# Kernel tuning notes

Measured on AMD Instinct MI355X. Metric: run time of the kernel, lower is better.

The kernel has to match this reference:

```python
import jax, jax.numpy as jnp
import numpy as np

NB = 4096      # num_batch
NUM = 128      # trajectory samples (P rows)
NVAR = 16      # polynomial coeffs (P cols)
NOBS = 10      # obstacles
NL, NU = 4, 8  # num_lower, num_upper
NPART = NU - NL
T_FIN = 10.0
A_OBS, B_OBS = 6.0, 3.2
RHO_INEQ = RHO_OBS = RHO_LANE = 1.0
V_MIN, V_MAX, A_MAX = 0.1, 30.0, 18.0
MAXITER = 30
W_SM = 100.0


def setup_inputs() -> dict:
    key = jax.random.key(0)
    ks = jax.random.split(key, 13)
    f = jnp.float32
    return {
        'P': jax.random.normal(ks[0], (NUM, NVAR), f),
        'Pdot': jax.random.normal(ks[1], (NUM, NVAR), f),
        'Pddot': jax.random.normal(ks[2], (NUM, NVAR), f),
        'init_state_ego': jax.random.normal(ks[3], (NB, 4), f),
        'fin_state_ego': jax.random.normal(ks[4], (NB, 3), f),
        'closest_obs': jax.random.normal(ks[5], (NB, 2 * NOBS), f),
        'v_obs': jax.random.normal(ks[6], (NB, 2 * NOBS), f),
        'y_ub': jax.random.uniform(ks[7], (NB,), f),
        'y_lb': jax.random.normal(ks[8], (NB,), f),
        'lamda_x': jax.random.normal(ks[9], (NB, NVAR), f),
        'lamda_y': jax.random.normal(ks[10], (NB, NVAR), f),
        'c_x_partial': jax.random.normal(ks[11], (NB, NPART), f),
        'c_y_partial': jax.random.normal(ks[12], (NB, NPART), f),
    }


def _forward(P, Pdot, Pddot, init_state_ego, fin_state_ego, closest_obs, v_obs,
             y_ub, y_lb, lamda_x, lamda_y, c_x_partial, c_y_partial):
    num, nvar = P.shape
    tot_time = jnp.linspace(0.0, T_FIN, num)
    eye = jnp.eye(nvar, dtype=P.dtype)
    A_part = eye[NL:NU]
    A_eq_x = jnp.vstack([P[0], Pdot[0], Pddot[0], Pdot[-1], A_part])            # [4+NPART, nvar]
    A_eq_y = jnp.vstack([P[0], Pdot[0], Pddot[0], P[-1], Pdot[-1], A_part])     # [5+NPART, nvar]
    cost_sm = W_SM * (Pddot.T @ Pddot + 0.1 * eye)
    A_vel, A_acc = Pdot, Pddot
    A_obs_mat = jnp.tile(P, (NOBS, 1))            # [NOBS*num, nvar]
    A_lane = jnp.vstack([P, -P])                  # [2*num, nvar]

    def kkt_inv(cost, A_eq):
        m = A_eq.shape[0]
        top = jnp.hstack([cost, A_eq.T])
        bot = jnp.hstack([A_eq, jnp.zeros((m, m), cost.dtype)])
        return jnp.linalg.inv(jnp.vstack([top, bot]))

    # --- obstacle trajectories: [B, NOBS*num] ---
    x_obs = closest_obs[:, :NOBS]; y_obs = closest_obs[:, NOBS:2 * NOBS]
    vx_obs = v_obs[:, :NOBS];      vy_obs = v_obs[:, NOBS:2 * NOBS]
    x_obs_traj = (x_obs[:, :, None] + vx_obs[:, :, None] * tot_time).reshape(NB, NOBS * num)
    y_obs_traj = (y_obs[:, :, None] + vy_obs[:, :, None] * tot_time).reshape(NB, NOBS * num)

    # --- boundary vectors ---
    x_init = init_state_ego[:, 0:1]; y_init = init_state_ego[:, 1:2]
    v_init = init_state_ego[:, 2:3]; psi_init = init_state_ego[:, 3:4]
    vx_init = v_init * jnp.cos(psi_init); vy_init = v_init * jnp.sin(psi_init)
    zc = jnp.zeros((NB, 1), P.dtype)
    x_fin = fin_state_ego[:, 0:1]; y_fin = fin_state_ego[:, 1:2]
    vx_fin = jnp.clip(fin_state_ego[:, 2:3], V_MIN, V_MAX)  # computed as in original (unused in b_eq)
    b_eq_x = jnp.hstack([x_init, vx_init, zc, x_fin, c_x_partial])
    b_eq_y = jnp.hstack([y_init, vy_init, zc, y_fin, zc, c_y_partial])

    # --- initialization QP (lincost = 0) ---
    cmi_x0 = kkt_inv(cost_sm, A_eq_x)
    cmi_y0 = kkt_inv(cost_sm, A_eq_y)
    sol_x0 = jnp.hstack([jnp.zeros((NB, nvar), P.dtype), b_eq_x]) @ cmi_x0.T
    sol_y0 = jnp.hstack([jnp.zeros((NB, nvar), P.dtype), b_eq_y]) @ cmi_y0.T
    primal_sol = jnp.hstack([sol_x0[:, :nvar], sol_y0[:, :nvar]])

    # --- optimizer KKT inverses ---
    cost_x = cost_sm + RHO_INEQ * (A_acc.T @ A_acc) + RHO_INEQ * (A_vel.T @ A_vel) + RHO_OBS * (A_obs_mat.T @ A_obs_mat)
    cost_y = cost_x + RHO_LANE * (A_lane.T @ A_lane)
    cmi_x = kkt_inv(cost_x, A_eq_x)
    cmi_y = kkt_inv(cost_y, A_eq_y)

    ones_num = jnp.ones((NB, num), P.dtype)
    b_lane = jnp.hstack([y_ub[:, None] * ones_num, -y_lb[:, None] * ones_num])  # [B, 2*num]

    def step(carry, _):
        primal, lx, ly = carry
        cx, cy = primal[:, :nvar], primal[:, nvar:]
        x, xdot, xddot = cx @ P.T, cx @ Pdot.T, cx @ Pddot.T      # [B, num]
        y, ydot, yddot = cy @ P.T, cy @ Pdot.T, cy @ Pddot.T

        wc = jnp.tile(x, (1, NOBS)) - x_obs_traj                   # [B, NOBS*num]
        ws = jnp.tile(y, (1, NOBS)) - y_obs_traj
        alpha_obs = jnp.arctan2(ws * A_OBS, wc * B_OBS)
        co, so = jnp.cos(alpha_obs), jnp.sin(alpha_obs)
        c1 = RHO_OBS * (A_OBS ** 2 * co ** 2 + B_OBS ** 2 * so ** 2)
        c2 = RHO_OBS * (A_OBS * wc * co + B_OBS * ws * so)
        d_obs = jnp.maximum(1.0, c2 / c1)

        alpha_v = jnp.arctan2(ydot, xdot)
        cv, sv = jnp.cos(alpha_v), jnp.sin(alpha_v)
        d_v = jnp.clip(RHO_INEQ * (xdot * cv + ydot * sv) / (RHO_INEQ * (cv ** 2 + sv ** 2)), V_MIN, V_MAX)

        alpha_a = jnp.arctan2(yddot, xddot)
        ca, sa = jnp.cos(alpha_a), jnp.sin(alpha_a)
        d_a = jnp.clip(RHO_INEQ * (xddot * ca + yddot * sa) / (RHO_INEQ * (ca ** 2 + sa ** 2)), 0.0, A_MAX)

        Ay = cy @ A_lane.T                                         # [B, 2*num]
        s_lane = jnp.maximum(0.0, -Ay + b_lane)
        res_lane = Ay - b_lane + s_lane
        res_ax, res_ay = xddot - d_a * ca, yddot - d_a * sa
        res_vx, res_vy = xdot - d_v * cv, ydot - d_v * sv
        res_xo, res_yo = wc - A_OBS * d_obs * co, ws - B_OBS * d_obs * so

        lx = lx - RHO_INEQ * (res_ax @ A_acc) - RHO_INEQ * (res_vx @ A_vel) - RHO_OBS * (res_xo @ A_obs_mat)
        ly = ly - RHO_INEQ * (res_ay @ A_acc) - RHO_INEQ * (res_vy @ A_vel) \
                - RHO_OBS * (res_yo @ A_obs_mat) - RHO_LANE * (res_lane @ A_lane)

        tmp_xo = x_obs_traj + A_OBS * d_obs * co
        tmp_yo = y_obs_traj + B_OBS * d_obs * so
        lincost_x = -lx - RHO_OBS * (tmp_xo @ A_obs_mat) - RHO_INEQ * ((d_a * ca) @ A_acc) - RHO_INEQ * ((d_v * cv) @ A_vel)
        lincost_y = -ly - RHO_OBS * (tmp_yo @ A_obs_mat) - RHO_INEQ * ((d_a * sa) @ A_acc) - RHO_INEQ * ((d_v * sv) @ A_vel) \
                    - RHO_LANE * ((b_lane - s_lane) @ A_lane)
        sol_x = jnp.hstack([-lincost_x, b_eq_x]) @ cmi_x.T
        sol_y = jnp.hstack([-lincost_y, b_eq_y]) @ cmi_y.T
        primal = jnp.hstack([sol_x[:, :nvar], sol_y[:, :nvar]])
        return (primal, lx, ly), None

    (primal_sol, lamda_x, lamda_y), _ = jax.lax.scan(step, (primal_sol, lamda_x, lamda_y), None, length=MAXITER)
    return primal_sol


def reference(P, Pdot, Pddot, init_state_ego, fin_state_ego, closest_obs, v_obs,
              y_ub, y_lb, lamda_x, lamda_y, c_x_partial, c_y_partial):
    return _forward(P, Pdot, Pddot, init_state_ego, fin_state_ego, closest_obs, v_obs,
                    y_ub, y_lb, lamda_x, lamda_y, c_x_partial, c_y_partial)
```

## Files before the change

kernel.cpp:

```cpp
#include <hip/hip_runtime.h>
#include <math.h>

#define NBATCH 4096
#define TNUM   128
#define NOBSC  10
#define MAXIT  30

#define WS_MX   0
#define WS_MY   256
#define WS_MGX  512
#define WS_MGY  768
#define WS_NX   1024
#define WS_NY   1152
#define WS_NX0  1296
#define WS_NY0  1424

#define RSTRIDE 132

typedef float f32x2 __attribute__((ext_vector_type(2)));
union F4 { float4 v; float f[4]; };

__device__ __forceinline__ f32x2 pfma(f32x2 a, f32x2 b, f32x2 c) {
  return __builtin_elementwise_fma(a, b, c);
}

__global__ __launch_bounds__(64) void planner_setup(
    const float* __restrict__ P, const float* __restrict__ Pd, const float* __restrict__ Pdd,
    float* __restrict__ ws)
{
  const int mid = blockIdx.x;
  const int tid = threadIdx.x;
  __shared__ double C[16][16];
  __shared__ double G[16][16];
  __shared__ double Ae[9][16];
  __shared__ double aug[25][50];
  __shared__ int pivs;

  const bool isY = (mid & 1);
  const int  m   = isY ? 9 : 8;
  const int  n   = 16 + m;
  const int  w   = 2 * n;

  for (int e = tid; e < 256; e += 64) {
    const int j = e >> 4, k = e & 15;
    double gdd = 0.0, gd = 0.0, g0 = 0.0;
    for (int t = 0; t < TNUM; ++t) {
      gdd += (double)Pdd[t*16+j] * (double)Pdd[t*16+k];
      gd  += (double)Pd [t*16+j] * (double)Pd [t*16+k];
      g0  += (double)P  [t*16+j] * (double)P  [t*16+k];
    }
    const double cs = 100.0 * (gdd + ((j == k) ? 0.1 : 0.0));
    const double g  = gdd + gd + (isY ? 12.0 : 10.0) * g0;
    G[j][k] = g;
    C[j][k] = (mid >= 2) ? (cs + g) : cs;
  }
  if (tid < 16) {
    const int j = tid;
    Ae[0][j] = (double)P  [0*16+j];
    Ae[1][j] = (double)Pd [0*16+j];
    Ae[2][j] = (double)Pdd[0*16+j];
    if (!isY) {
      Ae[3][j] = (double)Pd[127*16+j];
      for (int r = 4; r < 8; ++r) Ae[r][j] = (j == r) ? 1.0 : 0.0;
    } else {
      Ae[3][j] = (double)P [127*16+j];
      Ae[4][j] = (double)Pd[127*16+j];
      for (int r = 5; r < 9; ++r) Ae[r][j] = (j == (r-1)) ? 1.0 : 0.0;
    }
  }
  __syncthreads();

  for (int e = tid; e < n * w; e += 64) {
    const int r = e / w, c = e % w;
    double val;
    if (c < n) {
      if (r < 16) val = (c < 16) ? C[r][c] : Ae[c-16][r];
      else        val = (c < 16) ? Ae[r-16][c] : 0.0;
    } else {
      val = ((c - n) == r) ? 1.0 : 0.0;
    }
    aug[r][c] = val;
  }
  __syncthreads();

  for (int k = 0; k < n; ++k) {
    if (tid == 0) {
      int p = k; double best = fabs(aug[k][k]);
      for (int r = k+1; r < n; ++r) { double a = fabs(aug[r][k]); if (a > best) { best = a; p = r; } }
      pivs = p;
    }
    __syncthreads();
    const int p = pivs;
    if (p != k) {
      for (int c = tid; c < w; c += 64) { double t = aug[k][c]; aug[k][c] = aug[p][c]; aug[p][c] = t; }
    }
    __syncthreads();
    const double ipiv = 1.0 / aug[k][k];
    for (int c = tid; c < w; c += 64) aug[k][c] *= ipiv;
    __syncthreads();
    for (int r = tid; r < n; r += 64) {
      if (r != k) {
        const double f = aug[r][k];
        for (int c = k; c < w; ++c) aug[r][c] -= f * aug[k][c];
      }
    }
    __syncthreads();
  }

  if (mid == 0) {
    for (int e = tid; e < 16*8; e += 64) ws[WS_NX0 + e] = (float)aug[e >> 3][n + 16 + (e & 7)];
  } else if (mid == 1) {
    for (int e = tid; e < 16*9; e += 64) ws[WS_NY0 + e] = (float)aug[e / 9][n + 16 + (e % 9)];
  } else if (mid == 2) {
    for (int e = tid; e < 256;  e += 64) ws[WS_MX + e] = (float)aug[e >> 4][n + (e & 15)];
    for (int e = tid; e < 16*8; e += 64) ws[WS_NX + e] = (float)aug[e >> 3][n + 16 + (e & 7)];
  } else {
    for (int e = tid; e < 256;  e += 64) ws[WS_MY + e] = (float)aug[e >> 4][n + (e & 15)];
    for (int e = tid; e < 16*9; e += 64) ws[WS_NY + e] = (float)aug[e / 9][n + 16 + (e % 9)];
  }

  if (mid >= 2) {
    for (int e = tid; e < 256; e += 64) {
      const int j = e >> 4, k = e & 15;
      double s = 0.0;
      for (int mm = 0; mm < 16; ++mm) s += aug[j][n + mm] * G[mm][k];
      ws[(mid == 2 ? WS_MGX : WS_MGY) + e] = (float)s;
    }
  }
}

__global__ __launch_bounds__(128, 2) void planner_main(
    const float* __restrict__ P, const float* __restrict__ Pd, const float* __restrict__ Pdd,
    const float* __restrict__ init_state, const float* __restrict__ fin_state,
    const float* __restrict__ cobs, const float* __restrict__ vobs,
    const float* __restrict__ yub_g, const float* __restrict__ ylb_g,
    const float* __restrict__ lamx_g, const float* __restrict__ lamy_g,
    const float* __restrict__ cxp_g, const float* __restrict__ cyp_g,
    const float* __restrict__ ws, float* __restrict__ out)
{
  const int b    = blockIdx.x;
  const int tid  = threadIdx.x;
  const int lane = tid & 63;
  const int wv   = tid >> 6;
  const int r32  = lane & 31;
  const int rr   = tid & 15;
  const int side = (tid >> 4) & 1;

  __shared__ alignas(16) float red[32*RSTRIDE];
  __shared__ alignas(16) float cLw[2][32];
  __shared__ alignas(16) float hLw[2][32];
  __shared__ float pL[2][32];

  f32x2 Pr2[8], Pdr2[8], Pddr2[8];
  #pragma unroll
  for (int q = 0; q < 4; ++q) {
    F4 a, bb, cc;
    a.v  = *reinterpret_cast<const float4*>(P   + tid*16 + 4*q);
    bb.v = *reinterpret_cast<const float4*>(Pd  + tid*16 + 4*q);
    cc.v = *reinterpret_cast<const float4*>(Pdd + tid*16 + 4*q);
    Pr2  [2*q+0] = f32x2{a.f[0],  a.f[1]};  Pr2  [2*q+1] = f32x2{a.f[2],  a.f[3]};
    Pdr2 [2*q+0] = f32x2{bb.f[0], bb.f[1]}; Pdr2 [2*q+1] = f32x2{bb.f[2], bb.f[3]};
    Pddr2[2*q+0] = f32x2{cc.f[0], cc.f[1]}; Pddr2[2*q+1] = f32x2{cc.f[2], cc.f[3]};
  }

  f32x2 xot2[5], yot2[5];
  {
    const float tt = (float)tid * (10.0f/127.0f);
    #pragma unroll
    for (int o5 = 0; o5 < 5; ++o5) {
      const int o = 2*o5;
      xot2[o5] = f32x2{3.2f * fmaf(vobs[b*20+o],      tt, cobs[b*20+o]),
                       3.2f * fmaf(vobs[b*20+o+1],    tt, cobs[b*20+o+1])};
      yot2[o5] = f32x2{6.0f * fmaf(vobs[b*20+10+o],   tt, cobs[b*20+10+o]),
                       6.0f * fmaf(vobs[b*20+11+o],   tt, cobs[b*20+11+o])};
    }
  }
  const float yub = yub_g[b], ylb = ylb_g[b];

  float lam = (r32 < 16) ? lamx_g[b*16 + r32] : lamy_g[b*16 + (r32 - 16)];

  float constv, myc;
  {
    float beq[9];
    const float vi  = init_state[b*4+2];
    const float psi = init_state[b*4+3];
    if (side == 0) {
      beq[0] = init_state[b*4+0];
      beq[1] = vi * cosf(psi);
      beq[2] = 0.f;
      beq[3] = fin_state[b*3+0];
      #pragma unroll
      for (int i2 = 0; i2 < 4; ++i2) beq[4+i2] = cxp_g[b*4+i2];
      beq[8] = 0.f;
    } else {
      beq[0] = init_state[b*4+1];
      beq[1] = vi * sinf(psi);
      beq[2] = 0.f;
      beq[3] = fin_state[b*3+1];
      beq[4] = 0.f;
      #pragma unroll
      for (int i2 = 0; i2 < 4; ++i2) beq[5+i2] = cyp_g[b*4+i2];
    }
    const int nstr = side ? 9 : 8;
    const float* Np  = ws + (side ? WS_NY  : WS_NX ) + rr*nstr;
    const float* N0p = ws + (side ? WS_NY0 : WS_NX0) + rr*nstr;
    float cv = 0.f, c0 = 0.f;
    #pragma unroll
    for (int mm = 0; mm < 9; ++mm) {
      const float bm = beq[mm];
      cv = fmaf(Np[mm],  bm, cv);
      c0 = fmaf(N0p[mm], bm, c0);
    }
    constv = cv;
    myc    = c0;
    if (lane < 32) cLw[wv][lane] = c0;
  }

  const float* Mrow  = ws + (side ? WS_MY  : WS_MX ) + rr*16;
  const float* MGrow = ws + (side ? WS_MGY : WS_MGX) + rr*16;

  #pragma unroll 1
  for (int it = 0; it < MAXIT; ++it) {
    f32x2 xv{}, yv{}, xdv{}, ydv{}, xddv{}, yddv{};
    #pragma unroll
    for (int q = 0; q < 4; ++q) {
      F4 cx4, cy4;
      cx4.v = *reinterpret_cast<const float4*>(&cLw[wv][4*q]);
      cy4.v = *reinterpret_cast<const float4*>(&cLw[wv][16 + 4*q]);
      const f32x2 c01 = f32x2{cx4.f[0], cx4.f[1]}, c23 = f32x2{cx4.f[2], cx4.f[3]};
      const f32x2 d01 = f32x2{cy4.f[0], cy4.f[1]}, d23 = f32x2{cy4.f[2], cy4.f[3]};
      xv   = pfma(Pr2  [2*q], c01, xv);   xv   = pfma(Pr2  [2*q+1], c23, xv);
      yv   = pfma(Pr2  [2*q], d01, yv);   yv   = pfma(Pr2  [2*q+1], d23, yv);
      xdv  = pfma(Pdr2 [2*q], c01, xdv);  xdv  = pfma(Pdr2 [2*q+1], c23, xdv);
      ydv  = pfma(Pdr2 [2*q], d01, ydv);  ydv  = pfma(Pdr2 [2*q+1], d23, ydv);
      xddv = pfma(Pddr2[2*q], c01, xddv); xddv = pfma(Pddr2[2*q+1], c23, xddv);
      yddv = pfma(Pddr2[2*q], d01, yddv); yddv = pfma(Pddr2[2*q+1], d23, yddv);
    }
    const float x   = xv.x   + xv.y,   y   = yv.x   + yv.y;
    const float xd  = xdv.x  + xdv.y,  yd  = ydv.x  + ydv.y;
    const float xdd = xddv.x + xddv.y, ydd = yddv.x + yddv.y;

    const float ria = rsqrtf(fmaxf(fmaf(xdd, xdd, ydd*ydd), 1e-36f));
    const float ga1 = 1.0f - fminf(1.0f, 18.0f * ria);
    const float riv = rsqrtf(fmaxf(fmaf(xd, xd, yd*yd), 1e-36f));
    const float gv1 = 1.0f - fminf(fmaxf(1.0f, 0.1f*riv), 30.0f*riv);

    f32x2 Sx2{}, Sy2{};
    {
      const float t32 = 3.2f * x, t6 = 6.0f * y;
      const f32x2 xbb = f32x2{t32, t32}, ybb = f32x2{t6, t6};
      #pragma unroll
      for (int o5 = 0; o5 < 5; ++o5) {
        const f32x2 bw = xbb - xot2[o5];
        const f32x2 aw = ybb - yot2[o5];
        f32x2 r2 = pfma(bw, bw, aw*aw);
        const float e0 = fmaxf(fmaf(19.2f, rsqrtf(fmaxf(r2.x, 1e-36f)), -1.0f), 0.f);
        const float e1 = fmaxf(fmaf(19.2f, rsqrtf(fmaxf(r2.y, 1e-36f)), -1.0f), 0.f);
        const f32x2 ee = f32x2{e0, e1};
        Sx2 = pfma(ee, bw, Sx2);
        Sy2 = pfma(ee, aw, Sy2);
      }
    }
    const float Sxp = Sx2.x + Sx2.y, Syp = Sy2.x + Sy2.y;
    const float c0p = -Sxp * 0.3125f;
    const float rln = fmaxf(y - yub, 0.f) - fmaxf(ylb - y, 0.f);
    const float c2p = rln - Syp * (1.0f/6.0f);
    const float c0dd = xdd * ga1, c0d = xd * gv1;
    const float c2dd = ydd * ga1, c2d = yd * gv1;

    {
      const f32x2 A0 = f32x2{c0dd, c0dd}, D0 = f32x2{c0d, c0d}, Q0 = f32x2{c0p, c0p};
      const f32x2 A2 = f32x2{c2dd, c2dd}, D2 = f32x2{c2d, c2d}, Q2 = f32x2{c2p, c2p};
      float* col = red + tid;
      #pragma unroll
      for (int j2 = 0; j2 < 8; ++j2) {
        const f32x2 vx = pfma(A0, Pddr2[j2], pfma(D0, Pdr2[j2], Q0 * Pr2[j2]));
        const f32x2 vy = pfma(A2, Pddr2[j2], pfma(D2, Pdr2[j2], Q2 * Pr2[j2]));
        col[(2*j2  )*RSTRIDE] = vx.x;
        col[(2*j2+1)*RSTRIDE] = vx.y;
        col[(16+2*j2)*RSTRIDE] = vy.x;
        col[(17+2*j2)*RSTRIDE] = vy.y;
      }
    }
    __syncthreads();

    float h;
    {
      const int qq = tid >> 5;
      const float* rb = red + r32*RSTRIDE + (qq & 1)*32 + wv*64;
      f32x2 sA{}, sB{};
      #pragma unroll
      for (int mch = 0; mch < 8; ++mch) {
        F4 t;
        t.v = *reinterpret_cast<const float4*>(rb + 4*mch);
        sA += f32x2{t.f[0], t.f[1]};
        sB += f32x2{t.f[2], t.f[3]};
      }
      const f32x2 sAB = sA + sB;
      float s = sAB.x + sAB.y;
      s += __shfl_xor(s, 32);
      if (lane < 32) pL[wv][lane] = s;
      __syncthreads();

      const float S = s + pL[wv ^ 1][r32];
      lam -= S;
      h = lam - S;
      if (lane < 32) hLw[wv][lane] = h;
    }

    {
      f32x2 accv{};
      #pragma unroll
      for (int q = 0; q < 4; ++q) {
        F4 m4, g4, h4, c4;
        m4.v = *reinterpret_cast<const float4*>(Mrow  + 4*q);
        g4.v = *reinterpret_cast<const float4*>(MGrow + 4*q);
        h4.v = *reinterpret_cast<const float4*>(&hLw[wv][side*16 + 4*q]);
        c4.v = *reinterpret_cast<const float4*>(&cLw[wv][side*16 + 4*q]);
        accv = pfma(f32x2{m4.f[0], m4.f[1]}, f32x2{h4.f[0], h4.f[1]}, accv);
        accv = pfma(f32x2{g4.f[0], g4.f[1]}, f32x2{c4.f[0], c4.f[1]}, accv);
        accv = pfma(f32x2{m4.f[2], m4.f[3]}, f32x2{h4.f[2], h4.f[3]}, accv);
        accv = pfma(f32x2{g4.f[2], g4.f[3]}, f32x2{c4.f[2], c4.f[3]}, accv);
      }
      myc = constv + accv.x + accv.y;
      if (lane < 32) cLw[wv][lane] = myc;
    }
  }

  if (tid < 32) out[b*32 + tid] = myc;
}

extern "C" void kernel_launch(void* const* d_in, const int* in_sizes, int n_in,
                              void* d_out, int out_size, void* d_ws, size_t ws_size,
                              hipStream_t stream) {
  const float* P    = (const float*)d_in[0];
  const float* Pd   = (const float*)d_in[1];
  const float* Pdd  = (const float*)d_in[2];
  const float* init = (const float*)d_in[3];
  const float* fin  = (const float*)d_in[4];
  const float* cobs = (const float*)d_in[5];
  const float* vobs = (const float*)d_in[6];
  const float* yub  = (const float*)d_in[7];
  const float* ylb  = (const float*)d_in[8];
  const float* lamx = (const float*)d_in[9];
  const float* lamy = (const float*)d_in[10];
  const float* cxp  = (const float*)d_in[11];
  const float* cyp  = (const float*)d_in[12];
  float* ws  = (float*)d_ws;
  float* o   = (float*)d_out;

  planner_setup<<<dim3(4), dim3(64), 0, stream>>>(P, Pd, Pdd, ws);
  planner_main<<<dim3(NBATCH), dim3(128), 0, stream>>>(
      P, Pd, Pdd, init, fin, cobs, vobs, yub, ylb, lamx, lamy, cxp, cyp, ws, o);
}
```

Measured before the change: 240.6 us.

## Process two batch elements per block to reuse register-resident P matrices

```diff
diff --git a/kernel.cpp b/kernel.cpp
--- a/kernel.cpp
+++ b/kernel.cpp
@@ -138,7 +138,8 @@
     const float* __restrict__ cxp_g, const float* __restrict__ cyp_g,
     const float* __restrict__ ws, float* __restrict__ out)
 {
-  const int b    = blockIdx.x;
+  const int b0   = blockIdx.x * 2;
+  const int b1   = b0 + 1;
   const int tid  = threadIdx.x;
   const int lane = tid & 63;
   const int wv   = tid >> 6;
@@ -146,10 +147,14 @@
   const int rr   = tid & 15;
   const int side = (tid >> 4) & 1;
 
-  __shared__ alignas(16) float red[32*RSTRIDE];
-  __shared__ alignas(16) float cLw[2][32];
-  __shared__ alignas(16) float hLw[2][32];
-  __shared__ float pL[2][32];
+  __shared__ alignas(16) float redA[32*RSTRIDE];
+  __shared__ alignas(16) float redB[32*RSTRIDE];
+  __shared__ alignas(16) float cLwA[2][32];
+  __shared__ alignas(16) float cLwB[2][32];
+  __shared__ alignas(16) float hLwA[2][32];
+  __shared__ alignas(16) float hLwB[2][32];
+  __shared__ float pLA[2][32];
+  __shared__ float pLB[2][32];
 
   f32x2 Pr2[8], Pdr2[8], Pddr2[8];
   #pragma unroll
@@ -163,57 +168,95 @@
     Pddr2[2*q+0] = f32x2{cc.f[0], cc.f[1]}; Pddr2[2*q+1] = f32x2{cc.f[2], cc.f[3]};
   }
 
-  f32x2 xot2[5], yot2[5];
+  f32x2 xot2A[5], yot2A[5], xot2B[5], yot2B[5];
   {
     const float tt = (float)tid * (10.0f/127.0f);
     #pragma unroll
     for (int o5 = 0; o5 < 5; ++o5) {
       const int o = 2*o5;
-      xot2[o5] = f32x2{3.2f * fmaf(vobs[b*20+o],      tt, cobs[b*20+o]),
-                       3.2f * fmaf(vobs[b*20+o+1],    tt, cobs[b*20+o+1])};
-      yot2[o5] = f32x2{6.0f * fmaf(vobs[b*20+10+o],   tt, cobs[b*20+10+o]),
-                       6.0f * fmaf(vobs[b*20+11+o],   tt, cobs[b*20+11+o])};
-    }
-  }
-  const float yub = yub_g[b], ylb = ylb_g[b];
-
-  float lam = (r32 < 16) ? lamx_g[b*16 + r32] : lamy_g[b*16 + (r32 - 16)];
-
-  float constv, myc;
+      xot2A[o5] = f32x2{3.2f * fmaf(vobs[b0*20+o],    tt, cobs[b0*20+o]),
+                        3.2f * fmaf(vobs[b0*20+o+1],  tt, cobs[b0*20+o+1])};
+      yot2A[o5] = f32x2{6.0f * fmaf(vobs[b0*20+10+o], tt, cobs[b0*20+10+o]),
+                        6.0f * fmaf(vobs[b0*20+11+o], tt, cobs[b0*20+11+o])};
+      xot2B[o5] = f32x2{3.2f * fmaf(vobs[b1*20+o],    tt, cobs[b1*20+o]),
+                        3.2f * fmaf(vobs[b1*20+o+1],  tt, cobs[b1*20+o+1])};
+      yot2B[o5] = f32x2{6.0f * fmaf(vobs[b1*20+10+o], tt, cobs[b1*20+10+o]),
+                        6.0f * fmaf(vobs[b1*20+11+o], tt, cobs[b1*20+11+o])};
+    }
+  }
+  const float yubA = yub_g[b0], ylbA = ylb_g[b0];
+  const float yubB = yub_g[b1], ylbB = ylb_g[b1];
+
+  float lamA = (r32 < 16) ? lamx_g[b0*16 + r32] : lamy_g[b0*16 + (r32 - 16)];
+  float lamB = (r32 < 16) ? lamx_g[b1*16 + r32] : lamy_g[b1*16 + (r32 - 16)];
+
+  float constvA, mycA, constvB, mycB;
   {
-    float beq[9];
-    const float vi  = init_state[b*4+2];
-    const float psi = init_state[b*4+3];
-    if (side == 0) {
-      beq[0] = init_state[b*4+0];
-      beq[1] = vi * cosf(psi);
-      beq[2] = 0.f;
-      beq[3] = fin_state[b*3+0];
-      #pragma unroll
-      for (int i2 = 0; i2 < 4; ++i2) beq[4+i2] = cxp_g[b*4+i2];
-      beq[8] = 0.f;
-    } else {
-      beq[0] = init_state[b*4+1];
-      beq[1] = vi * sinf(psi);
-      beq[2] = 0.f;
-      beq[3] = fin_state[b*3+1];
-      beq[4] = 0.f;
-      #pragma unroll
-      for (int i2 = 0; i2 < 4; ++i2) beq[5+i2] = cyp_g[b*4+i2];
-    }
     const int nstr = side ? 9 : 8;
     const float* Np  = ws + (side ? WS_NY  : WS_NX ) + rr*nstr;
     const float* N0p = ws + (side ? WS_NY0 : WS_NX0) + rr*nstr;
-    float cv = 0.f, c0 = 0.f;
-    #pragma unroll
-    for (int mm = 0; mm < 9; ++mm) {
-      const float bm = beq[mm];
-      cv = fmaf(Np[mm],  bm, cv);
-      c0 = fmaf(N0p[mm], bm, c0);
-    }
-    constv = cv;
-    myc    = c0;
-    if (lane < 32) cLw[wv][lane] = c0;
+
+    float beq[9];
+    {
+      const float vi  = init_state[b0*4+2];
+      const float psi = init_state[b0*4+3];
+      if (side == 0) {
+        beq[0] = init_state[b0*4+0];
+        beq[1] = vi * cosf(psi);
+        beq[2] = 0.f;
+        beq[3] = fin_state[b0*3+0];
+        #pragma unroll
+        for (int i2 = 0; i2 < 4; ++i2) beq[4+i2] = cxp_g[b0*4+i2];
+        beq[8] = 0.f;
+      } else {
+        beq[0] = init_state[b0*4+1];
+        beq[1] = vi * sinf(psi);
+        beq[2] = 0.f;
+        beq[3] = fin_state[b0*3+1];
+        beq[4] = 0.f;
+        #pragma unroll
+        for (int i2 = 0; i2 < 4; ++i2) beq[5+i2] = cyp_g[b0*4+i2];
+      }
+      float cv = 0.f, c0 = 0.f;
+      #pragma unroll
+      for (int mm = 0; mm < 9; ++mm) {
+        const float bm = beq[mm];
+        cv = fmaf(Np[mm],  bm, cv);
+        c0 = fmaf(N0p[mm], bm, c0);
+      }
+      constvA = cv;  mycA = c0;
+      if (lane < 32) cLwA[wv][lane] = c0;
+    }
+    {
+      const float vi  = init_state[b1*4+2];
+      const float psi = init_state[b1*4+3];
+      if (side == 0) {
+        beq[0] = init_state[b1*4+0];
+        beq[1] = vi * cosf(psi);
+        beq[2] = 0.f;
+        beq[3] = fin_state[b1*3+0];
+        #pragma unroll
+        for (int i2 = 0; i2 < 4; ++i2) beq[4+i2] = cxp_g[b1*4+i2];
+        beq[8] = 0.f;
+      } else {
+        beq[0] = init_state[b1*4+1];
+        beq[1] = vi * sinf(psi);
+        beq[2] = 0.f;
+        beq[3] = fin_state[b1*3+1];
+        beq[4] = 0.f;
+        #pragma unroll
+        for (int i2 = 0; i2 < 4; ++i2) beq[5+i2] = cyp_g[b1*4+i2];
+      }
+      float cv = 0.f, c0 = 0.f;
+      #pragma unroll
+      for (int mm = 0; mm < 9; ++mm) {
+        const float bm = beq[mm];
+        cv = fmaf(Np[mm],  bm, cv);
+        c0 = fmaf(N0p[mm], bm, c0);
+      }
+      constvB = cv;  mycB = c0;
+      if (lane < 32) cLwB[wv][lane] = c0;
+    }
   }
 
   const float* Mrow  = ws + (side ? WS_MY  : WS_MX ) + rr*16;
@@ -221,113 +264,176 @@
 
   #pragma unroll 1
   for (int it = 0; it < MAXIT; ++it) {
-    f32x2 xv{}, yv{}, xdv{}, ydv{}, xddv{}, yddv{};
+    f32x2 xvA{}, yvA{}, xdvA{}, ydvA{}, xddvA{}, yddvA{};
+    f32x2 xvB{}, yvB{}, xdvB{}, ydvB{}, xddvB{}, yddvB{};
     #pragma unroll
     for (int q = 0; q < 4; ++q) {
-      F4 cx4, cy4;
-      cx4.v = *reinterpret_cast<const float4*>(&cLw[wv][4*q]);
-      cy4.v = *reinterpret_cast<const float4*>(&cLw[wv][16 + 4*q]);
-      const f32x2 c01 = f32x2{cx4.f[0], cx4.f[1]}, c23 = f32x2{cx4.f[2], cx4.f[3]};
-      const f32x2 d01 = f32x2{cy4.f[0], cy4.f[1]}, d23 = f32x2{cy4.f[2], cy4.f[3]};
-      xv   = pfma(Pr2  [2*q], c01, xv);   xv   = pfma(Pr2  [2*q+1], c23, xv);
-      yv   = pfma(Pr2  [2*q], d01, yv);   yv   = pfma(Pr2  [2*q+1], d23, yv);
-      xdv  = pfma(Pdr2 [2*q], c01, xdv);  xdv  = pfma(Pdr2 [2*q+1], c23, xdv);
-      ydv  = pfma(Pdr2 [2*q], d01, ydv);  ydv  = pfma(Pdr2 [2*q+1], d23, ydv);
-      xddv = pfma(Pddr2[2*q], c01, xddv); xddv = pfma(Pddr2[2*q+1], c23, xddv);
-      yddv = pfma(Pddr2[2*q], d01, yddv); yddv = pfma(Pddr2[2*q+1], d23, yddv);
-    }
-    const float x   = xv.x   + xv.y,   y   = yv.x   + yv.y;
-    const float xd  = xdv.x  + xdv.y,  yd  = ydv.x  + ydv.y;
-    const float xdd = xddv.x + xddv.y, ydd = yddv.x + yddv.y;
-
-    const float ria = rsqrtf(fmaxf(fmaf(xdd, xdd, ydd*ydd), 1e-36f));
-    const float ga1 = 1.0f - fminf(1.0f, 18.0f * ria);
-    const float riv = rsqrtf(fmaxf(fmaf(xd, xd, yd*yd), 1e-36f));
-    const float gv1 = 1.0f - fminf(fmaxf(1.0f, 0.1f*riv), 30.0f*riv);
-
-    f32x2 Sx2{}, Sy2{};
-    {
-      const float t32 = 3.2f * x, t6 = 6.0f * y;
-      const f32x2 xbb = f32x2{t32, t32}, ybb = f32x2{t6, t6};
+      F4 cxa, cya, cxb, cyb;
+      cxa.v = *reinterpret_cast<const float4*>(&cLwA[wv][4*q]);
+      cya.v = *reinterpret_cast<const float4*>(&cLwA[wv][16 + 4*q]);
+      cxb.v = *reinterpret_cast<const float4*>(&cLwB[wv][4*q]);
+      cyb.v = *reinterpret_cast<const float4*>(&cLwB[wv][16 + 4*q]);
+      const f32x2 cA01 = f32x2{cxa.f[0], cxa.f[1]}, cA23 = f32x2{cxa.f[2], cxa.f[3]};
+      const f32x2 dA01 = f32x2{cya.f[0], cya.f[1]}, dA23 = f32x2{cya.f[2], cya.f[3]};
+      const f32x2 cB01 = f32x2{cxb.f[0], cxb.f[1]}, cB23 = f32x2{cxb.f[2], cxb.f[3]};
+      const f32x2 dB01 = f32x2{cyb.f[0], cyb.f[1]}, dB23 = f32x2{cyb.f[2], cyb.f[3]};
+      xvA   = pfma(Pr2  [2*q], cA01, xvA);   xvA   = pfma(Pr2  [2*q+1], cA23, xvA);
+      yvA   = pfma(Pr2  [2*q], dA01, yvA);   yvA   = pfma(Pr2  [2*q+1], dA23, yvA);
+      xdvA  = pfma(Pdr2 [2*q], cA01, xdvA);  xdvA  = pfma(Pdr2 [2*q+1], cA23, xdvA);
+      ydvA  = pfma(Pdr2 [2*q], dA01, ydvA);  ydvA  = pfma(Pdr2 [2*q+1], dA23, ydvA);
+      xddvA = pfma(Pddr2[2*q], cA01, xddvA); xddvA = pfma(Pddr2[2*q+1], cA23, xddvA);
+      yddvA = pfma(Pddr2[2*q], dA01, yddvA); yddvA = pfma(Pddr2[2*q+1], dA23, yddvA);
+      xvB   = pfma(Pr2  [2*q], cB01, xvB);   xvB   = pfma(Pr2  [2*q+1], cB23, xvB);
+      yvB   = pfma(Pr2  [2*q], dB01, yvB);   yvB   = pfma(Pr2  [2*q+1], dB23, yvB);
+      xdvB  = pfma(Pdr2 [2*q], cB01, xdvB);  xdvB  = pfma(Pdr2 [2*q+1], cB23, xdvB);
+      ydvB  = pfma(Pdr2 [2*q], dB01, ydvB);  ydvB  = pfma(Pdr2 [2*q+1], dB23, ydvB);
+      xddvB = pfma(Pddr2[2*q], cB01, xddvB); xddvB = pfma(Pddr2[2*q+1], cB23, xddvB);
+      yddvB = pfma(Pddr2[2*q], dB01, yddvB); yddvB = pfma(Pddr2[2*q+1], dB23, yddvB);
+    }
+    const float xA   = xvA.x   + xvA.y,   yA   = yvA.x   + yvA.y;
+    const float xdA  = xdvA.x  + xdvA.y,  ydA  = ydvA.x  + ydvA.y;
+    const float xddA = xddvA.x + xddvA.y, yddA = yddvA.x + yddvA.y;
+    const float xB   = xvB.x   + xvB.y,   yB   = yvB.x   + yvB.y;
+    const float xdB  = xdvB.x  + xdvB.y,  ydB  = ydvB.x  + ydvB.y;
+    const float xddB = xddvB.x + xddvB.y, yddB = yddvB.x + yddvB.y;
+
+    const float riaA = rsqrtf(fmaxf(fmaf(xddA, xddA, yddA*yddA), 1e-36f));
+    const float ga1A = 1.0f - fminf(1.0f, 18.0f * riaA);
+    const float rivA = rsqrtf(fmaxf(fmaf(xdA, xdA, ydA*ydA), 1e-36f));
+    const float gv1A = 1.0f - fminf(fmaxf(1.0f, 0.1f*rivA), 30.0f*rivA);
+    const float riaB = rsqrtf(fmaxf(fmaf(xddB, xddB, yddB*yddB), 1e-36f));
+    const float ga1B = 1.0f - fminf(1.0f, 18.0f * riaB);
+    const float rivB = rsqrtf(fmaxf(fmaf(xdB, xdB, ydB*ydB), 1e-36f));
+    const float gv1B = 1.0f - fminf(fmaxf(1.0f, 0.1f*rivB), 30.0f*rivB);
+
+    f32x2 Sx2A{}, Sy2A{}, Sx2B{}, Sy2B{};
+    {
+      const float t32A = 3.2f * xA, t6A = 6.0f * yA;
+      const float t32B = 3.2f * xB, t6B = 6.0f * yB;
+      const f32x2 xbA = f32x2{t32A, t32A}, ybA = f32x2{t6A, t6A};
+      const f32x2 xbB = f32x2{t32B, t32B}, ybB = f32x2{t6B, t6B};
       #pragma unroll
       for (int o5 = 0; o5 < 5; ++o5) {
-        const f32x2 bw = xbb - xot2[o5];
-        const f32x2 aw = ybb - yot2[o5];
-        f32x2 r2 = pfma(bw, bw, aw*aw);
-        const float e0 = fmaxf(fmaf(19.2f, rsqrtf(fmaxf(r2.x, 1e-36f)), -1.0f), 0.f);
-        const float e1 = fmaxf(fmaf(19.2f, rsqrtf(fmaxf(r2.y, 1e-36f)), -1.0f), 0.f);
-        const f32x2 ee = f32x2{e0, e1};
-        Sx2 = pfma(ee, bw, Sx2);
-        Sy2 = pfma(ee, aw, Sy2);
-      }
-    }
-    const float Sxp = Sx2.x + Sx2.y, Syp = Sy2.x + Sy2.y;
-    const float c0p = -Sxp * 0.3125f;
-    const float rln = fmaxf(y - yub, 0.f) - fmaxf(ylb - y, 0.f);
-    const float c2p = rln - Syp * (1.0f/6.0f);
-    const float c0dd = xdd * ga1, c0d = xd * gv1;
-    const float c2dd = ydd * ga1, c2d = yd * gv1;
-
-    {
-      const f32x2 A0 = f32x2{c0dd, c0dd}, D0 = f32x2{c0d, c0d}, Q0 = f32x2{c0p, c0p};
-      const f32x2 A2 = f32x2{c2dd, c2dd}, D2 = f32x2{c2d, c2d}, Q2 = f32x2{c2p, c2p};
-      float* col = red + tid;
+        const f32x2 bwA = xbA - xot2A[o5];
+        const f32x2 awA = ybA - yot2A[o5];
+        const f32x2 bwB = xbB - xot2B[o5];
+        const f32x2 awB = ybB - yot2B[o5];
+        f32x2 r2A = pfma(bwA, bwA, awA*awA);
+        f32x2 r2B = pfma(bwB, bwB, awB*awB);
+        const float e0A = fmaxf(fmaf(19.2f, rsqrtf(fmaxf(r2A.x, 1e-36f)), -1.0f), 0.f);
+        const float e1A = fmaxf(fmaf(19.2f, rsqrtf(fmaxf(r2A.y, 1e-36f)), -1.0f), 0.f);
+        const float e0B = fmaxf(fmaf(19.2f, rsqrtf(fmaxf(r2B.x, 1e-36f)), -1.0f), 0.f);
+        const float e1B = fmaxf(fmaf(19.2f, rsqrtf(fmaxf(r2B.y, 1e-36f)), -1.0f), 0.f);
+        const f32x2 eeA = f32x2{e0A, e1A};
+        const f32x2 eeB = f32x2{e0B, e1B};
+        Sx2A = pfma(eeA, bwA, Sx2A);
+        Sy2A = pfma(eeA, awA, Sy2A);
+        Sx2B = pfma(eeB, bwB, Sx2B);
+        Sy2B = pfma(eeB, awB, Sy2B);
+      }
+    }
+    const float SxpA = Sx2A.x + Sx2A.y, SypA = Sy2A.x + Sy2A.y;
+    const float SxpB = Sx2B.x + Sx2B.y, SypB = Sy2B.x + Sy2B.y;
+    const float c0pA = -SxpA * 0.3125f;
+    const float rlnA = fmaxf(yA - yubA, 0.f) - fmaxf(ylbA - yA, 0.f);
+    const float c2pA = rlnA - SypA * (1.0f/6.0f);
+    const float c0ddA = xddA * ga1A, c0dA = xdA * gv1A;
+    const float c2ddA = yddA * ga1A, c2dA = ydA * gv1A;
+    const float c0pB = -SxpB * 0.3125f;
+    const float rlnB = fmaxf(yB - yubB, 0.f) - fmaxf(ylbB - yB, 0.f);
+    const float c2pB = rlnB - SypB * (1.0f/6.0f);
+    const float c0ddB = xddB * ga1B, c0dB = xdB * gv1B;
+    const float c2ddB = yddB * ga1B, c2dB = ydB * gv1B;
+
+    {
+      const f32x2 A0A = f32x2{c0ddA, c0ddA}, D0A = f32x2{c0dA, c0dA}, Q0A = f32x2{c0pA, c0pA};
+      const f32x2 A2A = f32x2{c2ddA, c2ddA}, D2A = f32x2{c2dA, c2dA}, Q2A = f32x2{c2pA, c2pA};
+      const f32x2 A0B = f32x2{c0ddB, c0ddB}, D0B = f32x2{c0dB, c0dB}, Q0B = f32x2{c0pB, c0pB};
+      const f32x2 A2B = f32x2{c2ddB, c2ddB}, D2B = f32x2{c2dB, c2dB}, Q2B = f32x2{c2pB, c2pB};
+      float* colA = redA + tid;
+      float* colB = redB + tid;
       #pragma unroll
       for (int j2 = 0; j2 < 8; ++j2) {
-        const f32x2 vx = pfma(A0, Pddr2[j2], pfma(D0, Pdr2[j2], Q0 * Pr2[j2]));
-        const f32x2 vy = pfma(A2, Pddr2[j2], pfma(D2, Pdr2[j2], Q2 * Pr2[j2]));
-        col[(2*j2  )*RSTRIDE] = vx.x;
-        col[(2*j2+1)*RSTRIDE] = vx.y;
-        col[(16+2*j2)*RSTRIDE] = vy.x;
-        col[(17+2*j2)*RSTRIDE] = vy.y;
+        const f32x2 vxA = pfma(A0A, Pddr2[j2], pfma(D0A, Pdr2[j2], Q0A * Pr2[j2]));
+        const f32x2 vyA = pfma(A2A, Pddr2[j2], pfma(D2A, Pdr2[j2], Q2A * Pr2[j2]));
+        const f32x2 vxB = pfma(A0B, Pddr2[j2], pfma(D0B, Pdr2[j2], Q0B * Pr2[j2]));
+        const f32x2 vyB = pfma(A2B, Pddr2[j2], pfma(D2B, Pdr2[j2], Q2B * Pr2[j2]));
+        colA[(2*j2  )*RSTRIDE]  = vxA.x;
+        colA[(2*j2+1)*RSTRIDE]  = vxA.y;
+        colA[(16+2*j2)*RSTRIDE] = vyA.x;
+        colA[(17+2*j2)*RSTRIDE] = vyA.y;
+        colB[(2*j2  )*RSTRIDE]  = vxB.x;
+        colB[(2*j2+1)*RSTRIDE]  = vxB.y;
+        colB[(16+2*j2)*RSTRIDE] = vyB.x;
+        colB[(17+2*j2)*RSTRIDE] = vyB.y;
       }
     }
     __syncthreads();
 
-    float h;
-    {
-      const int qq = tid >> 5;
-      const float* rb = red + r32*RSTRIDE + (qq & 1)*32 + wv*64;
-      f32x2 sA{}, sB{};
+    float hA, hB;
+    {
+      const int chunk = (tid >> 5) * 32;
+      const float* rbA = redA + r32*RSTRIDE + chunk;
+      const float* rbB = redB + r32*RSTRIDE + chunk;
+      f32x2 sA1{}, sA2{}, sB1{}, sB2{};
       #pragma unroll
       for (int mch = 0; mch < 8; ++mch) {
-        F4 t;
-        t.v = *reinterpret_cast<const float4*>(rb + 4*mch);
-        sA += f32x2{t.f[0], t.f[1]};
-        sB += f32x2{t.f[2], t.f[3]};
-      }
-      const f32x2 sAB = sA + sB;
-      float s = sAB.x + sAB.y;
-      s += __shfl_xor(s, 32);
-      if (lane < 32) pL[wv][lane] = s;
+        F4 ta, tb;
+        ta.v = *reinterpret_cast<const float4*>(rbA + 4*mch);
+        tb.v = *reinterpret_cast<const float4*>(rbB + 4*mch);
+        sA1 += f32x2{ta.f[0], ta.f[1]};
+        sA2 += f32x2{ta.f[2], ta.f[3]};
+        sB1 += f32x2{tb.f[0], tb.f[1]};
+        sB2 += f32x2{tb.f[2], tb.f[3]};
+      }
+      const f32x2 sAv = sA1 + sA2;
+      const f32x2 sBv = sB1 + sB2;
+      float sA = sAv.x + sAv.y;
+      float sB = sBv.x + sBv.y;
+      sA += __shfl_xor(sA, 32);
+      sB += __shfl_xor(sB, 32);
+      if (lane < 32) { pLA[wv][lane] = sA; pLB[wv][lane] = sB; }
       __syncthreads();
 
-      const float S = s + pL[wv ^ 1][r32];
-      lam -= S;
-      h = lam - S;
-      if (lane < 32) hLw[wv][lane] = h;
-    }
-
-    {
-      f32x2 accv{};
+      const float SA = sA + pLA[wv ^ 1][r32];
+      const float SB = sB + pLB[wv ^ 1][r32];
+      lamA -= SA;
+      lamB -= SB;
+      hA = lamA - SA;
+      hB = lamB - SB;
+      if (lane < 32) { hLwA[wv][lane] = hA; hLwB[wv][lane] = hB; }
+    }
+
+    {
+      f32x2 accA{}, accB{};
       #pragma unroll
       for (int q = 0; q < 4; ++q) {
-        F4 m4, g4, h4, c4;
-        m4.v = *reinterpret_cast<const float4*>(Mrow  + 4*q);
-        g4.v = *reinterpret_cast<const float4*>(MGrow + 4*q);
-        h4.v = *reinterpret_cast<const float4*>(&hLw[wv][side*16 + 4*q]);
-        c4.v = *reinterpret_cast<const float4*>(&cLw[wv][side*16 + 4*q]);
-        accv = pfma(f32x2{m4.f[0], m4.f[1]}, f32x2{h4.f[0], h4.f[1]}, accv);
-        accv = pfma(f32x2{g4.f[0], g4.f[1]}, f32x2{c4.f[0], c4.f[1]}, accv);
-        accv = pfma(f32x2{m4.f[2], m4.f[3]}, f32x2{h4.f[2], h4.f[3]}, accv);
-        accv = pfma(f32x2{g4.f[2], g4.f[3]}, f32x2{c4.f[2], c4.f[3]}, accv);
-      }
-      myc = constv + accv.x + accv.y;
-      if (lane < 32) cLw[wv][lane] = myc;
-    }
-  }
-
-  if (tid < 32) out[b*32 + tid] = myc;
+        F4 m4, g4, hA4, cA4, hB4, cB4;
+        m4.v  = *reinterpret_cast<const float4*>(Mrow  + 4*q);
+        g4.v  = *reinterpret_cast<const float4*>(MGrow + 4*q);
+        hA4.v = *reinterpret_cast<const float4*>(&hLwA[wv][side*16 + 4*q]);
+        cA4.v = *reinterpret_cast<const float4*>(&cLwA[wv][side*16 + 4*q]);
+        hB4.v = *reinterpret_cast<const float4*>(&hLwB[wv][side*16 + 4*q]);
+        cB4.v = *reinterpret_cast<const float4*>(&cLwB[wv][side*16 + 4*q]);
+        const f32x2 m01 = f32x2{m4.f[0], m4.f[1]}, m23 = f32x2{m4.f[2], m4.f[3]};
+        const f32x2 g01 = f32x2{g4.f[0], g4.f[1]}, g23 = f32x2{g4.f[2], g4.f[3]};
+        accA = pfma(m01, f32x2{hA4.f[0], hA4.f[1]}, accA);
+        accA = pfma(g01, f32x2{cA4.f[0], cA4.f[1]}, accA);
+        accA = pfma(m23, f32x2{hA4.f[2], hA4.f[3]}, accA);
+        accA = pfma(g23, f32x2{cA4.f[2], cA4.f[3]}, accA);
+        accB = pfma(m01, f32x2{hB4.f[0], hB4.f[1]}, accB);
+        accB = pfma(g01, f32x2{cB4.f[0], cB4.f[1]}, accB);
+        accB = pfma(m23, f32x2{hB4.f[2], hB4.f[3]}, accB);
+        accB = pfma(g23, f32x2{cB4.f[2], cB4.f[3]}, accB);
+      }
+      mycA = constvA + accA.x + accA.y;
+      mycB = constvB + accB.x + accB.y;
+      if (lane < 32) { cLwA[wv][lane] = mycA; cLwB[wv][lane] = mycB; }
+    }
+  }
+
+  if (tid < 32)      out[b0*32 + tid]        = mycA;
+  else if (tid < 64) out[b1*32 + (tid - 32)] = mycB;
 }
 
 extern "C" void kernel_launch(void* const* d_in, const int* in_sizes, int n_in,
@@ -350,6 +456,6 @@
   float* o   = (float*)d_out;
 
   planner_setup<<<dim3(4), dim3(64), 0, stream>>>(P, Pd, Pdd, ws);
-  planner_main<<<dim3(NBATCH), dim3(128), 0, stream>>>(
+  planner_main<<<dim3(NBATCH/2), dim3(128), 0, stream>>>(
       P, Pd, Pdd, init, fin, cobs, vobs, yub, ylb, lamx, lamy, cxp, cyp, ws, o);
 }
```

After: 261.2 us. +8.6%, slower.
